# Kernel tuning notes

Hardware: AMD Instinct MI355X
Metric: run time of the kernel (lower is better)

Reference implementation:

```python
import jax, jax.numpy as jnp
import numpy as np

N = 50000      # nodes
E = 600000     # edges
IN = 128       # input_dim
HID = 128      # hidden_dim
OUT = 128      # output_dim
H = 4          # heads
D = OUT // H   # head dim
R = 4          # rel_num
L = 2          # n_layer
M = 10000      # len(idx)
EPS = 1e-5


def setup_inputs() -> dict:
    key = jax.random.key(0)
    ks = jax.random.split(key, 16)
    f = jax.random.normal
    inp = {
        "x": f(ks[0], (N, IN), jnp.float32),
        "proj_w": f(ks[1], (IN, HID), jnp.float32) / np.sqrt(IN).astype(np.float32),
        "proj_b": jnp.zeros((HID,), jnp.float32),
        "bn_gamma": jnp.ones((HID,), jnp.float32),
        "bn_beta": jnp.zeros((HID,), jnp.float32),
        # per-layer HGTConv params (stacked on leading L axis; layer0 in=HID, layer1 in=OUT, equal here)
        "q_w": f(ks[2], (L, HID, OUT), jnp.float32) / np.sqrt(HID).astype(np.float32),
        "q_b": jnp.zeros((L, OUT), jnp.float32),
        "k_w": f(ks[3], (L, HID, OUT), jnp.float32) / np.sqrt(HID).astype(np.float32),
        "k_b": jnp.zeros((L, OUT), jnp.float32),
        "v_w": f(ks[4], (L, HID, OUT), jnp.float32) / np.sqrt(HID).astype(np.float32),
        "v_b": jnp.zeros((L, OUT), jnp.float32),
        "a_w": f(ks[5], (L, OUT, OUT), jnp.float32) / np.sqrt(OUT).astype(np.float32),
        "a_b": jnp.zeros((L, OUT), jnp.float32),
        "skip": jnp.ones((L,), jnp.float32),
        "a_rel": f(ks[6], (L, R, H, D, D), jnp.float32) / np.sqrt(D).astype(np.float32),
        "m_rel": f(ks[7], (L, R, H, D, D), jnp.float32) / np.sqrt(D).astype(np.float32),
        "p_rel": jnp.ones((L, R, H), jnp.float32),
        "edge_index": jax.random.randint(ks[8], (2, E), 0, N, dtype=jnp.int32),
        "edge_type": jax.random.randint(ks[9], (E,), 0, R, dtype=jnp.int32),
        "idx": jax.random.randint(ks[10], (M,), 0, N, dtype=jnp.int32),
    }
    return inp


def _hgt_forward(x, proj_w, proj_b, bn_gamma, bn_beta, q_w, q_b, k_w, k_b, v_w, v_b,
                 a_w, a_b, skip, a_rel, m_rel, p_rel, edge_index, edge_type, idx):
    # proj + BatchNorm1d (training-mode batch statistics, biased variance)
    h = x @ proj_w + proj_b
    mu = h.mean(axis=0)
    var = jnp.mean((h - mu) ** 2, axis=0)
    h = (h - mu) * jax.lax.rsqrt(var + EPS) * bn_gamma + bn_beta

    src, dst = edge_index[0], edge_index[1]          # message from src(j) to dst(i)
    seg = dst * R + edge_type                        # per-(dst, relation) softmax segments
    scale = np.float32(1.0 / np.sqrt(D))

    for l in range(L):
        q = (h @ q_w[l] + q_b[l]).reshape(N, H, D)
        k = (h @ k_w[l] + k_b[l]).reshape(N, H, D)
        v = (h @ v_w[l] + v_b[l]).reshape(N, H, D)
        # relation-specific key/value transforms for every node/relation: [N,R,H,D]
        k_all = jnp.einsum('nhd,rhde->nrhe', k, a_rel[l])
        v_all = jnp.einsum('nhd,rhde->nrhe', v, m_rel[l])
        k_e = k_all[src, edge_type]                  # [E,H,D]
        v_e = v_all[src, edge_type]                  # [E,H,D]
        score = jnp.sum(q[dst] * k_e, axis=-1) * p_rel[l][edge_type] * scale  # [E,H]
        # per-relation segment softmax over incoming edges of each dst node
        smax = jax.ops.segment_max(score, seg, num_segments=N * R)
        e = jnp.exp(score - smax[seg])
        denom = jax.ops.segment_sum(e, seg, num_segments=N * R)
        alpha = e / denom[seg]                        # [E,H]
        out = jax.ops.segment_sum(alpha[..., None] * v_e, dst, num_segments=N)
        out = out.reshape(N, OUT)
        out = jax.nn.gelu(out, approximate=False) @ a_w[l] + a_b[l]
        b = jax.nn.sigmoid(skip[l])                   # learned skip gate
        h = b * out + (1.0 - b) * h                   # dims match -> residual mix
    return h[idx]


def reference(x, proj_w, proj_b, bn_gamma, bn_beta, q_w, q_b, k_w, k_b, v_w, v_b,
              a_w, a_b, skip, a_rel, m_rel, p_rel, edge_index, edge_type, idx):
    return _hgt_forward(x, proj_w, proj_b, bn_gamma, bn_beta, q_w, q_b, k_w, k_b,
                        v_w, v_b, a_w, a_b, skip, a_rel, m_rel, p_rel,
                        edge_index, edge_type, idx)
```

## Files before the change

kernel.cpp:

```cpp
#include <hip/hip_runtime.h>
#include <math.h>

#define NN 50000
#define EE 600000
#define MOUT 10000
#define DEGCAP 384
#define NT4 (NN * 4)

typedef short bf16x8 __attribute__((ext_vector_type(8)));
typedef float f32x4 __attribute__((ext_vector_type(4)));

__device__ __forceinline__ unsigned short f2bf(float x) {
    unsigned int u = __float_as_uint(x);
    u = (u + 0x7FFFu + ((u >> 16) & 1u)) >> 16;
    return (unsigned short)u;
}
__device__ __forceinline__ float bf2f(unsigned int b) {
    return __uint_as_float(b << 16);
}
__device__ __forceinline__ uint4 pack8bf(float4 a, float4 b) {
    uint4 r;
    r.x = (unsigned int)f2bf(a.x) | ((unsigned int)f2bf(a.y) << 16);
    r.y = (unsigned int)f2bf(a.z) | ((unsigned int)f2bf(a.w) << 16);
    r.z = (unsigned int)f2bf(b.x) | ((unsigned int)f2bf(b.y) << 16);
    r.w = (unsigned int)f2bf(b.z) | ((unsigned int)f2bf(b.w) << 16);
    return r;
}

__global__ __launch_bounds__(256) void prep_kernel(
    const float* __restrict__ proj_w, const float* __restrict__ a_w,
    const float* __restrict__ q_w, const float* __restrict__ q_b,
    const float* __restrict__ a_rel,
    const float* __restrict__ k_w, const float* __restrict__ k_b,
    const float* __restrict__ v_w, const float* __restrict__ v_b,
    const float* __restrict__ m_rel, const float* __restrict__ p_rel,
    unsigned short* __restrict__ wt_pa, unsigned short* __restrict__ qkvw,
    float* __restrict__ fbias, unsigned short* __restrict__ msg_wt,
    int* __restrict__ cnt, float* __restrict__ stats)
{
    const int b = blockIdx.x, t = threadIdx.x;
    if (b < 192) {
        int wi = b >> 6;
        int flat = (b & 63) * 256 + t;
        int n = flat >> 7, c = flat & 127;
        const float* src = (wi == 0) ? proj_w : (wi == 1) ? a_w : a_w + 16384;
        wt_pa[(size_t)wi * 16384 + n * 128 + c] = f2bf(src[c * 128 + n]);
    } else if (b < 960) {
        int q = b - 192;
        int l = q >= 384 ? 1 : 0;
        int flat = (q - l * 384) * 256 + t;
        int nrow = flat >> 7, c = flat & 127;
        unsigned short* wt = qkvw + (size_t)l * 98304;
        float* fb = fbias + l * 768;
        if (nrow < 512) {
            int r = nrow >> 7, hh = (nrow >> 5) & 3, d = nrow & 31;
            float prl = p_rel[l * 16 + r * 4 + hh] * 0.17677669529663687f;
            const float* qwc = q_w + (size_t)l * 16384 + c * 128 + hh * 32;
            const float* ar  = a_rel + (size_t)(l * 4 + r) * 4096 + hh * 1024 + d * 32;
            float s = 0.f;
            #pragma unroll 8
            for (int e = 0; e < 32; ++e) s += qwc[e] * ar[e];
            wt[(size_t)nrow * 128 + c] = f2bf(s * prl);
            if (c == 0) {
                const float* qb = q_b + l * 128 + hh * 32;
                float bb = 0.f;
                #pragma unroll 8
                for (int e = 0; e < 32; ++e) bb += qb[e] * ar[e];
                fb[nrow] = bb * prl;
            }
        } else {
            int j = nrow - 512;
            int tt = j >> 3, s = j & 7;
            int col = 4 * tt + (s & 3);
            const float* w  = (s < 4) ? k_w : v_w;
            const float* bb = (s < 4) ? k_b : v_b;
            wt[(size_t)nrow * 128 + c] = f2bf(w[(size_t)l * 16384 + c * 128 + col]);
            if (c == 0) fb[nrow] = bb[l * 128 + col];
        }
    } else if (b < 1472) {
        int q = b - 960;
        int l = q >= 256 ? 1 : 0;
        int flat = (q - l * 256) * 256 + t;
        int n = flat >> 9, kk = flat & 511;
        int h = n >> 5, e = n & 31;
        int r = kk >> 7, h2 = (kk >> 5) & 3, d = kk & 31;
        float val = (h2 == h) ? m_rel[(size_t)(l * 4 + r) * 4096 + h * 1024 + d * 32 + e] : 0.f;
        msg_wt[(size_t)l * 65536 + (size_t)n * 512 + kk] = f2bf(val);
    } else {
        int i = (b - 1472) * 256 + t;
        if (i < NT4) cnt[i] = 0;
        if (i < 256) stats[i] = 0.f;
    }
}

__global__ __launch_bounds__(256) void hist_kernel(const int* __restrict__ ei,
    const int* __restrict__ et, int* __restrict__ cnt, int E)
{
    int e = blockIdx.x * 256 + threadIdx.x;
    if (e < E) atomicAdd(&cnt[ei[E + e] * 4 + et[e]], 1);
}

__global__ __launch_bounds__(256) void scan_block_kernel(const int* __restrict__ cnt,
    int* __restrict__ excl, int* __restrict__ bsum, int n)
{
    __shared__ int tmp[256];
    int i = blockIdx.x * 256 + threadIdx.x;
    int v = (i < n) ? cnt[i] : 0;
    tmp[threadIdx.x] = v;
    __syncthreads();
    for (int ofs = 1; ofs < 256; ofs <<= 1) {
        int t = (threadIdx.x >= ofs) ? tmp[threadIdx.x - ofs] : 0;
        __syncthreads();
        tmp[threadIdx.x] += t;
        __syncthreads();
    }
    if (i < n) excl[i] = tmp[threadIdx.x] - v;
    if (threadIdx.x == 255) bsum[blockIdx.x] = tmp[255];
}

__global__ __launch_bounds__(256) void scan_add_kernel(int* __restrict__ excl,
    const int* __restrict__ bsum, int* __restrict__ fill,
    int* __restrict__ maskz, int n, int total)
{
    __shared__ int red[256];
    const int b = blockIdx.x;
    int partial = 0;
    for (int j = threadIdx.x; j < b; j += 256) partial += bsum[j];
    red[threadIdx.x] = partial;
    __syncthreads();
    for (int ofs = 128; ofs > 0; ofs >>= 1) {
        if (threadIdx.x < ofs) red[threadIdx.x] += red[threadIdx.x + ofs];
        __syncthreads();
    }
    int prefix = red[0];
    int i = b * 256 + threadIdx.x;
    if (i < n) {
        int o = excl[i] + prefix;
        excl[i] = o;
        fill[i] = o;
    }
    if (i < 12500) maskz[i] = 0;
    if (b == 0 && threadIdx.x == 0) excl[n] = total;
}

__global__ __launch_bounds__(256) void scatter_kernel(const int* __restrict__ ei,
    const int* __restrict__ et, int* __restrict__ fill, int* __restrict__ pack,
    const int* __restrict__ idxp, unsigned char* __restrict__ mask, int Mo, int E)
{
    int e = blockIdx.x * 256 + threadIdx.x;
    if (e >= E) return;
    int seg = ei[E + e] * 4 + et[e];
    int p = atomicAdd(&fill[seg], 1);
    pack[p] = ei[e];
    if (e < Mo) mask[idxp[e]] = 1;
}

__global__ __launch_bounds__(256) void projstats_kernel(
    const float* __restrict__ X, const unsigned short* __restrict__ Wt,
    const float* __restrict__ bias, unsigned short* __restrict__ Cb,
    float* __restrict__ stats, int M)
{
    __shared__ unsigned short As[128 * 40];
    __shared__ unsigned short Bs[128 * 40];
    const int t = threadIdx.x;
    const int wave = t >> 6, lane = t & 63;
    const int quad = lane >> 4, l16 = lane & 15;
    const int row0 = blockIdx.x * 128;
    const int wr = (wave & 1) * 64, wc = (wave >> 1) * 64;
    const int sr = t >> 1, sc = (t & 1) * 16;
    const int grow = row0 + sr;

    f32x4 acc[4][4];
    #pragma unroll
    for (int i = 0; i < 4; ++i)
        #pragma unroll
        for (int j = 0; j < 4; ++j)
            acc[i][j] = (f32x4){0.f, 0.f, 0.f, 0.f};

    uint4 av0 = make_uint4(0,0,0,0), av1 = av0, bv0, bv1;
    if (grow < M) {
        const float4* ap = (const float4*)(X + (size_t)grow * 128 + sc);
        av0 = pack8bf(ap[0], ap[1]);
        av1 = pack8bf(ap[2], ap[3]);
    }
    {
        const uint4* bp = (const uint4*)(Wt + (size_t)sr * 128 + sc);
        bv0 = bp[0]; bv1 = bp[1];
    }
    for (int it = 0; it < 4; ++it) {
        __syncthreads();
        *(uint4*)(As + sr * 40 + sc)     = av0;
        *(uint4*)(As + sr * 40 + sc + 8) = av1;
        *(uint4*)(Bs + sr * 40 + sc)     = bv0;
        *(uint4*)(Bs + sr * 40 + sc + 8) = bv1;
        __syncthreads();
        if (it + 1 < 4) {
            int kb = (it + 1) * 32;
            if (grow < M) {
                const float4* ap = (const float4*)(X + (size_t)grow * 128 + kb + sc);
                av0 = pack8bf(ap[0], ap[1]);
                av1 = pack8bf(ap[2], ap[3]);
            }
            const uint4* bp = (const uint4*)(Wt + (size_t)sr * 128 + kb + sc);
            bv0 = bp[0]; bv1 = bp[1];
        }
        bf16x8 af[4], bfr[4];
        #pragma unroll
        for (int f = 0; f < 4; ++f) {
            af[f]  = *(const bf16x8*)(As + (wr + f * 16 + l16) * 40 + quad * 8);
            bfr[f] = *(const bf16x8*)(Bs + (wc + f * 16 + l16) * 40 + quad * 8);
        }
        #pragma unroll
        for (int fr = 0; fr < 4; ++fr)
            #pragma unroll
            for (int fc = 0; fc < 4; ++fc)
                acc[fr][fc] = __builtin_amdgcn_mfma_f32_16x16x32_bf16(
                    af[fr], bfr[fc], acc[fr][fc], 0, 0, 0);
    }

    #pragma unroll
    for (int fc = 0; fc < 4; ++fc) {
        const int col = wc + fc * 16 + l16;
        const float bv = bias[col];
        float s = 0.f, s2 = 0.f;
        #pragma unroll
        for (int fr = 0; fr < 4; ++fr)
            #pragma unroll
            for (int reg = 0; reg < 4; ++reg) {
                int row = row0 + wr + fr * 16 + quad * 4 + reg;
                float val = acc[fr][fc][reg] + bv;
                if (row < M) {
                    Cb[(size_t)row * 128 + col] = f2bf(val);
                    s += val; s2 += val * val;
                }
            }
        s  += __shfl_xor(s, 16);  s  += __shfl_xor(s, 32);
        s2 += __shfl_xor(s2, 16); s2 += __shfl_xor(s2, 32);
        if (quad == 0) {
            atomicAdd(&stats[col], s);
            atomicAdd(&stats[128 + col], s2);
        }
    }
}

__global__ __launch_bounds__(256) void bnqkv_kernel(
    const unsigned short* __restrict__ hb, const float* __restrict__ stats,
    const float* __restrict__ gamma, const float* __restrict__ beta,
    const unsigned short* __restrict__ qkvw, const float* __restrict__ fbias,
    unsigned short* __restrict__ hn, unsigned short* __restrict__ qkv, int M)
{
    __shared__ unsigned short hS[128 * 136];
    __shared__ unsigned short Bs[128 * 40];
    __shared__ float mulS[128], addS[128];
    const int t = threadIdx.x;
    const int row0 = blockIdx.x * 128;
    if (t < 128) {
        float invN = 1.f / 50000.f;
        float mu = stats[t] * invN;
        float var = stats[128 + t] * invN - mu * mu;
        float ml = rsqrtf(var + 1e-5f) * gamma[t];
        mulS[t] = ml;
        addS[t] = beta[t] - mu * ml;
    }
    __syncthreads();
    #pragma unroll
    for (int u = 0; u < 8; ++u) {
        int li = t + u * 256;
        int row = li >> 4, c0 = (li & 15) * 8;
        uint4 pk = make_uint4(0, 0, 0, 0);
        if (row0 + row < M)
            pk = ((const uint4*)(hb + (size_t)(row0 + row) * 128))[li & 15];
        unsigned int w[4] = {pk.x, pk.y, pk.z, pk.w};
        uint4 o;
        unsigned int ov[4];
        #pragma unroll
        for (int g = 0; g < 4; ++g) {
            int c = c0 + g * 2;
            float a0 = bf2f(w[g] & 0xFFFFu) * mulS[c]     + addS[c];
            float a1 = bf2f(w[g] >> 16)     * mulS[c + 1] + addS[c + 1];
            ov[g] = (unsigned int)f2bf(a0) | ((unsigned int)f2bf(a1) << 16);
        }
        o.x = ov[0]; o.y = ov[1]; o.z = ov[2]; o.w = ov[3];
        *(uint4*)(hS + row * 136 + c0) = o;
        if (row0 + row < M)
            ((uint4*)(hn + (size_t)(row0 + row) * 128))[li & 15] = o;
    }
    __syncthreads();

    const int wave = t >> 6, lane = t & 63;
    const int quad = lane >> 4, l16 = lane & 15;
    const int wr = (wave & 1) * 64, wcl = (wave >> 1) * 64;
    const int sr = t >> 1, scc = (t & 1) * 16;

    uint4 pv0, pv1;
    {
        const uint4* bp = (const uint4*)(qkvw + (size_t)sr * 128 + scc);
        pv0 = bp[0]; pv1 = bp[1];
    }
    for (int ch = 0; ch < 6; ++ch) {
        f32x4 acc[4][4];
        #pragma unroll
        for (int i = 0; i < 4; ++i)
            #pragma unroll
            for (int j = 0; j < 4; ++j)
                acc[i][j] = (f32x4){0.f, 0.f, 0.f, 0.f};
        for (int it = 0; it < 4; ++it) {
            __syncthreads();
            *(uint4*)(Bs + sr * 40 + scc)     = pv0;
            *(uint4*)(Bs + sr * 40 + scc + 8) = pv1;
            __syncthreads();
            int nit = it + 1, nch = ch;
            if (nit == 4) { nit = 0; ++nch; }
            if (nch < 6) {
                const uint4* bp = (const uint4*)(qkvw + (size_t)(nch * 128 + sr) * 128 + nit * 32 + scc);
                pv0 = bp[0]; pv1 = bp[1];
            }
            bf16x8 af[4], bfr[4];
            #pragma unroll
            for (int f = 0; f < 4; ++f) {
                af[f]  = *(const bf16x8*)(hS + (wr + f * 16 + l16) * 136 + it * 32 + quad * 8);
                bfr[f] = *(const bf16x8*)(Bs + (wcl + f * 16 + l16) * 40 + quad * 8);
            }
            #pragma unroll
            for (int fr = 0; fr < 4; ++fr)
                #pragma unroll
                for (int fc = 0; fc < 4; ++fc)
                    acc[fr][fc] = __builtin_amdgcn_mfma_f32_16x16x32_bf16(
                        af[fr], bfr[fc], acc[fr][fc], 0, 0, 0);
        }
        float b4[4];
        #pragma unroll
        for (int fc = 0; fc < 4; ++fc)
            b4[fc] = fbias[ch * 128 + wcl + fc * 16 + l16];
        #pragma unroll
        for (int fr = 0; fr < 4; ++fr)
            #pragma unroll
            for (int reg = 0; reg < 4; ++reg) {
                int row = row0 + wr + fr * 16 + quad * 4 + reg;
                if (row >= M) continue;
                #pragma unroll
                for (int fc = 0; fc < 4; ++fc) {
                    int col = ch * 128 + wcl + fc * 16 + l16;
                    qkv[(size_t)row * 768 + col] = f2bf(acc[fr][fc][reg] + b4[fc]);
                }
            }
    }
}

__global__ __launch_bounds__(256) void agg_fused_kernel(
    const unsigned short* __restrict__ qkv,
    const unsigned short* __restrict__ qbuf, int qpitch,
    const int* __restrict__ off4, const int* __restrict__ pack,
    const int* __restrict__ rowmap, unsigned short* __restrict__ aggb, int count)
{
    __shared__ int spack[4][DEGCAP];
    const int wv = threadIdx.x >> 6;
    const int lane = threadIdx.x & 63;
    const int l32 = lane & 31;
    const int hi = lane >> 5;
    const int unit = blockIdx.x * 4 + wv;
    if (unit >= count) return;
    const int node = rowmap ? __builtin_amdgcn_readfirstlane(rowmap[unit]) : unit;

    const uint2* qrow = (const uint2*)(qbuf + (size_t)unit * qpitch);
    uint2 quv[4];
    #pragma unroll
    for (int r = 0; r < 4; ++r) quv[r] = qrow[r * 32 + l32];

    int off_r[5];
    #pragma unroll
    for (int i = 0; i < 5; ++i)
        off_r[i] = __builtin_amdgcn_readfirstlane(off4[node * 4 + i]);
    const int beg = off_r[0];
    const int deg = off_r[4] - beg;
    const bool cached = deg <= DEGCAP;

    if (cached) {
        for (int i = lane; i < deg; i += 64) spack[wv][i] = pack[beg + i];
        asm volatile("s_waitcnt vmcnt(0) lgkmcnt(0)" ::: "memory");
    }

    uint2 outw[4];
    #pragma unroll
    for (int r = 0; r < 4; ++r) {
        float q0 = bf2f(quv[r].x & 0xFFFFu), q1 = bf2f(quv[r].x >> 16);
        float q2 = bf2f(quv[r].y & 0xFFFFu), q3 = bf2f(quv[r].y >> 16);
        float den = 0.f, a0 = 0.f, a1 = 0.f, a2 = 0.f, a3 = 0.f;

        if (cached) {
            const int rb = off_r[r] - beg, re = off_r[r + 1] - beg;
            for (int i = rb; i < re; i += 4) {
                int i0 = i + hi;      if (i0 >= re) i0 = re - 1;
                int i1 = i + 2 + hi;  if (i1 >= re) i1 = re - 1;
                int s0 = spack[wv][i0], s1 = spack[wv][i1];
                uint4 kv0 = *(const uint4*)(qkv + (size_t)s0 * 768 + 512 + l32 * 8);
                uint4 kv1 = *(const uint4*)(qkv + (size_t)s1 * 768 + 512 + l32 * 8);
                {
                    float p = q0 * bf2f(kv0.x & 0xFFFFu) + q1 * bf2f(kv0.x >> 16)
                            + q2 * bf2f(kv0.y & 0xFFFFu) + q3 * bf2f(kv0.y >> 16);
                    p += __shfl_xor(p, 1); p += __shfl_xor(p, 2); p += __shfl_xor(p, 4);
                    float e = __expf(fminf(fmaxf(p, -80.f), 80.f));
                    if (i + hi >= re) e = 0.f;
                    den += e;
                    a0 += e * bf2f(kv0.z & 0xFFFFu); a1 += e * bf2f(kv0.z >> 16);
                    a2 += e * bf2f(kv0.w & 0xFFFFu); a3 += e * bf2f(kv0.w >> 16);
                }
                {
                    float p = q0 * bf2f(kv1.x & 0xFFFFu) + q1 * bf2f(kv1.x >> 16)
                            + q2 * bf2f(kv1.y & 0xFFFFu) + q3 * bf2f(kv1.y >> 16);
                    p += __shfl_xor(p, 1); p += __shfl_xor(p, 2); p += __shfl_xor(p, 4);
                    float e = __expf(fminf(fmaxf(p, -80.f), 80.f));
                    if (i + 2 + hi >= re) e = 0.f;
                    den += e;
                    a0 += e * bf2f(kv1.z & 0xFFFFu); a1 += e * bf2f(kv1.z >> 16);
                    a2 += e * bf2f(kv1.w & 0xFFFFu); a3 += e * bf2f(kv1.w >> 16);
                }
            }
        } else {
            const int pe_end = off_r[r + 1];
            for (int pp = off_r[r]; pp < pe_end; pp += 2) {
                int pe = pp + hi; if (pe >= pe_end) pe = pe_end - 1;
                int src = pack[pe];
                uint4 kv = *(const uint4*)(qkv + (size_t)src * 768 + 512 + l32 * 8);
                float p = q0 * bf2f(kv.x & 0xFFFFu) + q1 * bf2f(kv.x >> 16)
                        + q2 * bf2f(kv.y & 0xFFFFu) + q3 * bf2f(kv.y >> 16);
                p += __shfl_xor(p, 1); p += __shfl_xor(p, 2); p += __shfl_xor(p, 4);
                float e = __expf(fminf(fmaxf(p, -80.f), 80.f));
                if (pp + hi >= pe_end) e = 0.f;
                den += e;
                a0 += e * bf2f(kv.z & 0xFFFFu); a1 += e * bf2f(kv.z >> 16);
                a2 += e * bf2f(kv.w & 0xFFFFu); a3 += e * bf2f(kv.w >> 16);
            }
        }
        den += __shfl_xor(den, 32);
        a0  += __shfl_xor(a0, 32);
        a1  += __shfl_xor(a1, 32);
        a2  += __shfl_xor(a2, 32);
        a3  += __shfl_xor(a3, 32);
        float inv = den > 0.f ? 1.f / den : 0.f;
        outw[r].x = (unsigned int)f2bf(a0 * inv) | ((unsigned int)f2bf(a1 * inv) << 16);
        outw[r].y = (unsigned int)f2bf(a2 * inv) | ((unsigned int)f2bf(a3 * inv) << 16);
    }
    if (hi == 0) {
        uint2* op = (uint2*)(aggb + (size_t)unit * 512);
        #pragma unroll
        for (int r = 0; r < 4; ++r) op[r * 32 + l32] = outw[r];
    }
}

__global__ __launch_bounds__(256) void mlpqkv_kernel(
    const unsigned short* __restrict__ A, const unsigned short* __restrict__ W3t,
    const unsigned short* __restrict__ AWt, const float* __restrict__ a_bias,
    const float* __restrict__ skipv, const unsigned short* __restrict__ hres,
    const unsigned short* __restrict__ qkvw1, const float* __restrict__ fbias1,
    const unsigned char* __restrict__ mask,
    unsigned short* __restrict__ h1, unsigned short* __restrict__ qkv, int M)
{
    __shared__ unsigned short As[128 * 40];
    __shared__ unsigned short Bs[128 * 40];
    __shared__ unsigned short msgS[128 * 136];
    const int t = threadIdx.x;
    const int wave = t >> 6, lane = t & 63;
    const int quad = lane >> 4, l16 = lane & 15;
    const int row0 = blockIdx.x * 128;
    const int wr = (wave & 1) * 64, wcl = (wave >> 1) * 64;
    const int sr = t >> 1, scc = (t & 1) * 16;
    const int grow = row0 + sr;
    const bool rvalid = grow < M;

    f32x4 acc[4][4];
    #pragma unroll
    for (int i = 0; i < 4; ++i)
        #pragma unroll
        for (int j = 0; j < 4; ++j)
            acc[i][j] = (f32x4){0.f, 0.f, 0.f, 0.f};

    uint4 av0 = make_uint4(0,0,0,0), av1 = av0, bv0, bv1;
    if (rvalid) {
        const uint4* ap = (const uint4*)(A + (size_t)grow * 512 + scc);
        av0 = ap[0]; av1 = ap[1];
    }
    {
        const uint4* bp = (const uint4*)(W3t + (size_t)sr * 512 + scc);
        bv0 = bp[0]; bv1 = bp[1];
    }
    for (int it = 0; it < 16; ++it) {
        __syncthreads();
        *(uint4*)(As + sr * 40 + scc)     = av0;
        *(uint4*)(As + sr * 40 + scc + 8) = av1;
        *(uint4*)(Bs + sr * 40 + scc)     = bv0;
        *(uint4*)(Bs + sr * 40 + scc + 8) = bv1;
        __syncthreads();
        if (it + 1 < 16) {
            int kb = (it + 1) * 32;
            if (rvalid) {
                const uint4* ap = (const uint4*)(A + (size_t)grow * 512 + kb + scc);
                av0 = ap[0]; av1 = ap[1];
            }
            const uint4* bp = (const uint4*)(W3t + (size_t)sr * 512 + kb + scc);
            bv0 = bp[0]; bv1 = bp[1];
        }
        bf16x8 af[4], bfr[4];
        #pragma unroll
        for (int f = 0; f < 4; ++f) {
            af[f]  = *(const bf16x8*)(As + (wr + f * 16 + l16) * 40 + quad * 8);
            bfr[f] = *(const bf16x8*)(Bs + (wcl + f * 16 + l16) * 40 + quad * 8);
        }
        #pragma unroll
        for (int fr = 0; fr < 4; ++fr)
            #pragma unroll
            for (int fc = 0; fc < 4; ++fc)
                acc[fr][fc] = __builtin_amdgcn_mfma_f32_16x16x32_bf16(
                    af[fr], bfr[fc], acc[fr][fc], 0, 0, 0);
    }

    #pragma unroll
    for (int fr = 0; fr < 4; ++fr)
        #pragma unroll
        for (int reg = 0; reg < 4; ++reg) {
            int rl = wr + fr * 16 + quad * 4 + reg;
            #pragma unroll
            for (int fc = 0; fc < 4; ++fc) {
                int col = wcl + fc * 16 + l16;
                float v = acc[fr][fc][reg];
                float gl = 0.5f * v * (1.f + erff(v * 0.70710678118654752f));
                msgS[rl * 136 + col] = f2bf(gl);
            }
        }

    f32x4 acc2[4][4];
    #pragma unroll
    for (int i = 0; i < 4; ++i)
        #pragma unroll
        for (int j = 0; j < 4; ++j)
            acc2[i][j] = (f32x4){0.f, 0.f, 0.f, 0.f};
    uint4 pv0, pv1;
    {
        const uint4* bp = (const uint4*)(AWt + (size_t)sr * 128 + scc);
        pv0 = bp[0]; pv1 = bp[1];
    }
    for (int it = 0; it < 4; ++it) {
        __syncthreads();
        *(uint4*)(Bs + sr * 40 + scc)     = pv0;
        *(uint4*)(Bs + sr * 40 + scc + 8) = pv1;
        __syncthreads();
        if (it + 1 < 4) {
            const uint4* bp = (const uint4*)(AWt + (size_t)sr * 128 + (it + 1) * 32 + scc);
            pv0 = bp[0]; pv1 = bp[1];
        } else {
            const uint4* bp = (const uint4*)(qkvw1 + (size_t)(4 * 128 + sr) * 128 + scc);
            pv0 = bp[0]; pv1 = bp[1];
        }
        bf16x8 af[4], bfr[4];
        #pragma unroll
        for (int f = 0; f < 4; ++f) {
            af[f]  = *(const bf16x8*)(msgS + (wr + f * 16 + l16) * 136 + it * 32 + quad * 8);
            bfr[f] = *(const bf16x8*)(Bs + (wcl + f * 16 + l16) * 40 + quad * 8);
        }
        #pragma unroll
        for (int fr = 0; fr < 4; ++fr)
            #pragma unroll
            for (int fc = 0; fc < 4; ++fc)
                acc2[fr][fc] = __builtin_amdgcn_mfma_f32_16x16x32_bf16(
                    af[fr], bfr[fc], acc2[fr][fc], 0, 0, 0);
    }

    const float gate = 1.f / (1.f + __expf(-skipv[0]));
    __syncthreads();
    #pragma unroll
    for (int fr = 0; fr < 4; ++fr)
        #pragma unroll
        for (int reg = 0; reg < 4; ++reg) {
            int rl = wr + fr * 16 + quad * 4 + reg;
            int row = row0 + rl;
            const bool rv = row < M;
            const bool mw = rv && mask[row];
            #pragma unroll
            for (int fc = 0; fc < 4; ++fc) {
                int col = wcl + fc * 16 + l16;
                float val = acc2[fr][fc][reg] + a_bias[col];
                float nv = val;
                if (rv) {
                    unsigned int hu = hres[(size_t)row * 128 + col];
                    nv = gate * val + (1.f - gate) * bf2f(hu);
                    if (mw) h1[(size_t)row * 128 + col] = f2bf(nv);
                }
                msgS[rl * 136 + col] = f2bf(nv);
            }
        }

    for (int ch = 4; ch < 6; ++ch) {
        f32x4 acc3[4][4];
        #pragma unroll
        for (int i = 0; i < 4; ++i)
            #pragma unroll
            for (int j = 0; j < 4; ++j)
                acc3[i][j] = (f32x4){0.f, 0.f, 0.f, 0.f};
        for (int it = 0; it < 4; ++it) {
            __syncthreads();
            *(uint4*)(Bs + sr * 40 + scc)     = pv0;
            *(uint4*)(Bs + sr * 40 + scc + 8) = pv1;
            __syncthreads();
            int nit = it + 1, nch = ch;
            if (nit == 4) { nit = 0; ++nch; }
            if (nch < 6) {
                const uint4* bp = (const uint4*)(qkvw1 + (size_t)(nch * 128 + sr) * 128 + nit * 32 + scc);
                pv0 = bp[0]; pv1 = bp[1];
            }
            bf16x8 af[4], bfr[4];
            #pragma unroll
            for (int f = 0; f < 4; ++f) {
                af[f]  = *(const bf16x8*)(msgS + (wr + f * 16 + l16) * 136 + it * 32 + quad * 8);
                bfr[f] = *(const bf16x8*)(Bs + (wcl + f * 16 + l16) * 40 + quad * 8);
            }
            #pragma unroll
            for (int fr = 0; fr < 4; ++fr)
                #pragma unroll
                for (int fc = 0; fc < 4; ++fc)
                    acc3[fr][fc] = __builtin_amdgcn_mfma_f32_16x16x32_bf16(
                        af[fr], bfr[fc], acc3[fr][fc], 0, 0, 0);
        }
        float b4[4];
        #pragma unroll
        for (int fc = 0; fc < 4; ++fc)
            b4[fc] = fbias1[ch * 128 + wcl + fc * 16 + l16];
        #pragma unroll
        for (int fr = 0; fr < 4; ++fr)
            #pragma unroll
            for (int reg = 0; reg < 4; ++reg) {
                int row = row0 + wr + fr * 16 + quad * 4 + reg;
                if (row >= M) continue;
                #pragma unroll
                for (int fc = 0; fc < 4; ++fc) {
                    int col = ch * 128 + wcl + fc * 16 + l16;
                    qkv[(size_t)row * 768 + col] = f2bf(acc3[fr][fc][reg] + b4[fc]);
                }
            }
    }
}

__global__ __launch_bounds__(256) void q1_kernel(
    const unsigned short* __restrict__ h1, const int* __restrict__ idxp,
    const unsigned short* __restrict__ qkvw1, const float* __restrict__ fbias1,
    unsigned short* __restrict__ q1, int M)
{
    __shared__ unsigned short hS[128 * 136];
    __shared__ unsigned short Bs[128 * 40];
    const int t = threadIdx.x;
    const int row0 = blockIdx.x * 128;
    #pragma unroll
    for (int u = 0; u < 8; ++u) {
        int li = t + u * 256;
        int row = li >> 4, c = li & 15;
        uint4 pk = make_uint4(0, 0, 0, 0);
        if (row0 + row < M) {
            int node = idxp[row0 + row];
            pk = ((const uint4*)(h1 + (size_t)node * 128))[c];
        }
        *(uint4*)(hS + row * 136 + c * 8) = pk;
    }
    __syncthreads();

    const int wave = t >> 6, lane = t & 63;
    const int quad = lane >> 4, l16 = lane & 15;
    const int wr = (wave & 1) * 64, wcl = (wave >> 1) * 64;
    const int sr = t >> 1, scc = (t & 1) * 16;
    uint4 pv0, pv1;
    {
        const uint4* bp = (const uint4*)(qkvw1 + (size_t)sr * 128 + scc);
        pv0 = bp[0]; pv1 = bp[1];
    }
    for (int ch = 0; ch < 4; ++ch) {
        f32x4 acc[4][4];
        #pragma unroll
        for (int i = 0; i < 4; ++i)
            #pragma unroll
            for (int j = 0; j < 4; ++j)
                acc[i][j] = (f32x4){0.f, 0.f, 0.f, 0.f};
        for (int it = 0; it < 4; ++it) {
            __syncthreads();
            *(uint4*)(Bs + sr * 40 + scc)     = pv0;
            *(uint4*)(Bs + sr * 40 + scc + 8) = pv1;
            __syncthreads();
            int nit = it + 1, nch = ch;
            if (nit == 4) { nit = 0; ++nch; }
            if (nch < 4) {
                const uint4* bp = (const uint4*)(qkvw1 + (size_t)(nch * 128 + sr) * 128 + nit * 32 + scc);
                pv0 = bp[0]; pv1 = bp[1];
            }
            bf16x8 af[4], bfr[4];
            #pragma unroll
            for (int f = 0; f < 4; ++f) {
                af[f]  = *(const bf16x8*)(hS + (wr + f * 16 + l16) * 136 + it * 32 + quad * 8);
                bfr[f] = *(const bf16x8*)(Bs + (wcl + f * 16 + l16) * 40 + quad * 8);
            }
            #pragma unroll
            for (int fr = 0; fr < 4; ++fr)
                #pragma unroll
                for (int fc = 0; fc < 4; ++fc)
                    acc[fr][fc] = __builtin_amdgcn_mfma_f32_16x16x32_bf16(
                        af[fr], bfr[fc], acc[fr][fc], 0, 0, 0);
        }
        float b4[4];
        #pragma unroll
        for (int fc = 0; fc < 4; ++fc)
            b4[fc] = fbias1[ch * 128 + wcl + fc * 16 + l16];
        #pragma unroll
        for (int fr = 0; fr < 4; ++fr)
            #pragma unroll
            for (int reg = 0; reg < 4; ++reg) {
                int row = row0 + wr + fr * 16 + quad * 4 + reg;
                if (row >= M) continue;
                #pragma unroll
                for (int fc = 0; fc < 4; ++fc) {
                    int col = ch * 128 + wcl + fc * 16 + l16;
                    q1[(size_t)row * 512 + col] = f2bf(acc[fr][fc][reg] + b4[fc]);
                }
            }
    }
}

__global__ __launch_bounds__(256) void mlp1_kernel(
    const unsigned short* __restrict__ A, const unsigned short* __restrict__ W3t,
    const unsigned short* __restrict__ AWt, const float* __restrict__ a_bias,
    const float* __restrict__ skipv, const unsigned short* __restrict__ hres,
    const int* __restrict__ rowmap, float* __restrict__ out, int M)
{
    __shared__ unsigned short As[128 * 40];
    __shared__ unsigned short Bs[128 * 40];
    __shared__ unsigned short msgS[128 * 136];
    const int t = threadIdx.x;
    const int wave = t >> 6, lane = t & 63;
    const int quad = lane >> 4, l16 = lane & 15;
    const int row0 = blockIdx.x * 128;
    const int wr = (wave & 1) * 64, wcl = (wave >> 1) * 64;
    const int sr = t >> 1, scc = (t & 1) * 16;
    const int grow = row0 + sr;
    const bool rvalid = grow < M;

    f32x4 acc[4][4];
    #pragma unroll
    for (int i = 0; i < 4; ++i)
        #pragma unroll
        for (int j = 0; j < 4; ++j)
            acc[i][j] = (f32x4){0.f, 0.f, 0.f, 0.f};

    uint4 av0 = make_uint4(0,0,0,0), av1 = av0, bv0, bv1;
    if (rvalid) {
        const uint4* ap = (const uint4*)(A + (size_t)grow * 512 + scc);
        av0 = ap[0]; av1 = ap[1];
    }
    {
        const uint4* bp = (const uint4*)(W3t + (size_t)sr * 512 + scc);
        bv0 = bp[0]; bv1 = bp[1];
    }
    for (int it = 0; it < 16; ++it) {
        __syncthreads();
        *(uint4*)(As + sr * 40 + scc)     = av0;
        *(uint4*)(As + sr * 40 + scc + 8) = av1;
        *(uint4*)(Bs + sr * 40 + scc)     = bv0;
        *(uint4*)(Bs + sr * 40 + scc + 8) = bv1;
        __syncthreads();
        if (it + 1 < 16) {
            int kb = (it + 1) * 32;
            if (rvalid) {
                const uint4* ap = (const uint4*)(A + (size_t)grow * 512 + kb + scc);
                av0 = ap[0]; av1 = ap[1];
            }
            const uint4* bp = (const uint4*)(W3t + (size_t)sr * 512 + kb + scc);
            bv0 = bp[0]; bv1 = bp[1];
        }
        bf16x8 af[4], bfr[4];
        #pragma unroll
        for (int f = 0; f < 4; ++f) {
            af[f]  = *(const bf16x8*)(As + (wr + f * 16 + l16) * 40 + quad * 8);
            bfr[f] = *(const bf16x8*)(Bs + (wcl + f * 16 + l16) * 40 + quad * 8);
        }
        #pragma unroll
        for (int fr = 0; fr < 4; ++fr)
            #pragma unroll
            for (int fc = 0; fc < 4; ++fc)
                acc[fr][fc] = __builtin_amdgcn_mfma_f32_16x16x32_bf16(
                    af[fr], bfr[fc], acc[fr][fc], 0, 0, 0);
    }

    #pragma unroll
    for (int fr = 0; fr < 4; ++fr)
        #pragma unroll
        for (int reg = 0; reg < 4; ++reg) {
            int rl = wr + fr * 16 + quad * 4 + reg;
            #pragma unroll
            for (int fc = 0; fc < 4; ++fc) {
                int col = wcl + fc * 16 + l16;
                float v = acc[fr][fc][reg];
                float gl = 0.5f * v * (1.f + erff(v * 0.70710678118654752f));
                msgS[rl * 136 + col] = f2bf(gl);
            }
        }

    f32x4 acc2[4][4];
    #pragma unroll
    for (int i = 0; i < 4; ++i)
        #pragma unroll
        for (int j = 0; j < 4; ++j)
            acc2[i][j] = (f32x4){0.f, 0.f, 0.f, 0.f};
    uint4 pv0, pv1;
    {
        const uint4* bp = (const uint4*)(AWt + (size_t)sr * 128 + scc);
        pv0 = bp[0]; pv1 = bp[1];
    }
    for (int it = 0; it < 4; ++it) {
        __syncthreads();
        *(uint4*)(Bs + sr * 40 + scc)     = pv0;
        *(uint4*)(Bs + sr * 40 + scc + 8) = pv1;
        __syncthreads();
        if (it + 1 < 4) {
            const uint4* bp = (const uint4*)(AWt + (size_t)sr * 128 + (it + 1) * 32 + scc);
            pv0 = bp[0]; pv1 = bp[1];
        }
        bf16x8 af[4], bfr[4];
        #pragma unroll
        for (int f = 0; f < 4; ++f) {
            af[f]  = *(const bf16x8*)(msgS + (wr + f * 16 + l16) * 136 + it * 32 + quad * 8);
            bfr[f] = *(const bf16x8*)(Bs + (wcl + f * 16 + l16) * 40 + quad * 8);
        }
        #pragma unroll
        for (int fr = 0; fr < 4; ++fr)
            #pragma unroll
            for (int fc = 0; fc < 4; ++fc)
                acc2[fr][fc] = __builtin_amdgcn_mfma_f32_16x16x32_bf16(
                    af[fr], bfr[fc], acc2[fr][fc], 0, 0, 0);
    }

    const float gate = 1.f / (1.f + __expf(-skipv[0]));
    #pragma unroll
    for (int fr = 0; fr < 4; ++fr)
        #pragma unroll
        for (int reg = 0; reg < 4; ++reg) {
            int row = row0 + wr + fr * 16 + quad * 4 + reg;
            if (row >= M) continue;
            int hrow = rowmap[row];
            #pragma unroll
            for (int fc = 0; fc < 4; ++fc) {
                int col = wcl + fc * 16 + l16;
                float val = acc2[fr][fc][reg] + a_bias[col];
                float nv = gate * val + (1.f - gate) * bf2f((unsigned int)hres[(size_t)hrow * 128 + col]);
                out[(size_t)row * 128 + col] = nv;
            }
        }
}

extern "C" void kernel_launch(void* const* d_in, const int* in_sizes, int n_in,
                              void* d_out, int out_size, void* d_ws, size_t ws_size,
                              hipStream_t stream)
{
    const float* x      = (const float*)d_in[0];
    const float* proj_w = (const float*)d_in[1];
    const float* proj_b = (const float*)d_in[2];
    const float* bn_g   = (const float*)d_in[3];
    const float* bn_b   = (const float*)d_in[4];
    const float* q_w    = (const float*)d_in[5];
    const float* q_b    = (const float*)d_in[6];
    const float* k_w    = (const float*)d_in[7];
    const float* k_b    = (const float*)d_in[8];
    const float* v_w    = (const float*)d_in[9];
    const float* v_b    = (const float*)d_in[10];
    const float* a_w    = (const float*)d_in[11];
    const float* a_b    = (const float*)d_in[12];
    const float* skip   = (const float*)d_in[13];
    const float* a_rel  = (const float*)d_in[14];
    const float* m_rel  = (const float*)d_in[15];
    const float* p_rel  = (const float*)d_in[16];
    const int* edge_index = (const int*)d_in[17];
    const int* edge_type  = (const int*)d_in[18];
    const int* idx        = (const int*)d_in[19];
    float* out = (float*)d_out;

    const int N = NN, E = EE;
    float* ws = (float*)d_ws;
    size_t o = 0;
    float* stats  = ws + o;  o += 256;
    float* fbias  = ws + o;  o += 2 * 768;
    int* cnt  = (int*)(ws + o); o += NT4;
    int* off4 = (int*)(ws + o); o += NT4 + 1;
    int* fill = (int*)(ws + o); o += NT4;
    int* bsum = (int*)(ws + o); o += 1024;
    int* pack = (int*)(ws + o); o += E;
    unsigned short* x_bf   = (unsigned short*)(ws + o); o += (size_t)N * 64;
    unsigned short* h_bf   = (unsigned short*)(ws + o); o += (size_t)N * 64;
    unsigned short* hn_bf  = (unsigned short*)(ws + o); o += (size_t)N * 64;
    unsigned short* h1_bf  = (unsigned short*)(ws + o); o += (size_t)N * 64;
    unsigned short* qkv_bf = (unsigned short*)(ws + o); o += (size_t)N * 384;
    unsigned short* agg_bf = (unsigned short*)(ws + o); o += (size_t)N * 256;
    unsigned short* wt_pa  = (unsigned short*)(ws + o); o += 3 * 16384 / 2;
    unsigned short* qkvw   = (unsigned short*)(ws + o); o += 2 * 98304 / 2;
    unsigned short* msg_wt = (unsigned short*)(ws + o); o += 2 * 65536 / 2;

    unsigned char* mask = (unsigned char*)cnt;
    unsigned short* q1 = x_bf;

    const int NB4 = (NT4 + 255) / 256;
    const int g = (N + 127) / 128;

    prep_kernel<<<1472 + NB4, 256, 0, stream>>>(
        proj_w, a_w, q_w, q_b, a_rel, k_w, k_b, v_w, v_b, m_rel, p_rel,
        wt_pa, qkvw, fbias, msg_wt, cnt, stats);

    hist_kernel<<<(E + 255) / 256, 256, 0, stream>>>(edge_index, edge_type, cnt, E);
    scan_block_kernel<<<NB4, 256, 0, stream>>>(cnt, off4, bsum, NT4);
    scan_add_kernel<<<NB4, 256, 0, stream>>>(off4, bsum, fill, cnt, NT4, E);
    scatter_kernel<<<(E + 255) / 256, 256, 0, stream>>>(edge_index, edge_type, fill,
                                                        pack, idx, mask, MOUT, E);

    projstats_kernel<<<g, 256, 0, stream>>>(x, wt_pa, proj_b, h_bf, stats, N);

    bnqkv_kernel<<<g, 256, 0, stream>>>(h_bf, stats, bn_g, bn_b, qkvw, fbias,
                                        hn_bf, qkv_bf, N);

    agg_fused_kernel<<<(N + 3) / 4, 256, 0, stream>>>(qkv_bf, qkv_bf, 768,
                                                      off4, pack, nullptr, agg_bf, N);

    mlpqkv_kernel<<<g, 256, 0, stream>>>(agg_bf, msg_wt, wt_pa + 16384, a_b, skip,
                                         hn_bf, qkvw + 98304, fbias + 768,
                                         mask, h1_bf, qkv_bf, N);

    q1_kernel<<<(MOUT + 127) / 128, 256, 0, stream>>>(h1_bf, idx, qkvw + 98304,
                                                      fbias + 768, q1, MOUT);

    agg_fused_kernel<<<(MOUT + 3) / 4, 256, 0, stream>>>(qkv_bf, q1, 512,
                                                         off4, pack, idx, agg_bf, MOUT);

    mlp1_kernel<<<(MOUT + 127) / 128, 256, 0, stream>>>(agg_bf, msg_wt + 65536,
                                                        wt_pa + 2 * 16384, a_b + 128,
                                                        skip + 1, h1_bf, idx, out, MOUT);
}
```

Baseline: 442.5 us.

## Exploit block-diagonal relation message weights to cut MFMA work fourfold

The message-transform GEMM used a dense 512x128 weight that was zero outside head-diagonal blocks. The new layout stores only the per-relation 128x32 compact blocks, and the GEMM loop runs 4 relation iterations of K=32 instead of 16. Each wave selects the A columns for its own heads from a full 128-column slab staged in shared memory, which removes the As buffer and three quarters of the MFMAs and weight loads. The cost is larger per-thread register staging (8 uint4 per iteration) and an extra barrier before the reused msgS buffer is overwritten.

```diff
diff --git a/kernel.cpp b/kernel.cpp
--- a/kernel.cpp
+++ b/kernel.cpp
@@ -77,17 +77,16 @@
             wt[(size_t)nrow * 128 + c] = f2bf(w[(size_t)l * 16384 + c * 128 + col]);
             if (c == 0) fb[nrow] = bb[l * 128 + col];
         }
-    } else if (b < 1472) {
+    } else if (b < 1088) {
         int q = b - 960;
-        int l = q >= 256 ? 1 : 0;
-        int flat = (q - l * 256) * 256 + t;
-        int n = flat >> 9, kk = flat & 511;
-        int h = n >> 5, e = n & 31;
-        int r = kk >> 7, h2 = (kk >> 5) & 3, d = kk & 31;
-        float val = (h2 == h) ? m_rel[(size_t)(l * 4 + r) * 4096 + h * 1024 + d * 32 + e] : 0.f;
-        msg_wt[(size_t)l * 65536 + (size_t)n * 512 + kk] = f2bf(val);
+        int l = q >= 64 ? 1 : 0;
+        int flat = (q - l * 64) * 256 + t;
+        int r = flat >> 12, rem = flat & 4095;
+        int n = rem >> 5, d = rem & 31;
+        float val = m_rel[(size_t)(l * 4 + r) * 4096 + (n >> 5) * 1024 + d * 32 + (n & 31)];
+        msg_wt[(size_t)l * 16384 + r * 4096 + n * 32 + d] = f2bf(val);
     } else {
-        int i = (b - 1472) * 256 + t;
+        int i = (b - 1088) * 256 + t;
         if (i < NT4) cnt[i] = 0;
         if (i < 256) stats[i] = 0.f;
     }
@@ -449,14 +448,13 @@
 }
 
 __global__ __launch_bounds__(256) void mlpqkv_kernel(
-    const unsigned short* __restrict__ A, const unsigned short* __restrict__ W3t,
+    const unsigned short* __restrict__ A, const unsigned short* __restrict__ W3c,
     const unsigned short* __restrict__ AWt, const float* __restrict__ a_bias,
     const float* __restrict__ skipv, const unsigned short* __restrict__ hres,
     const unsigned short* __restrict__ qkvw1, const float* __restrict__ fbias1,
     const unsigned char* __restrict__ mask,
     unsigned short* __restrict__ h1, unsigned short* __restrict__ qkv, int M)
 {
-    __shared__ unsigned short As[128 * 40];
     __shared__ unsigned short Bs[128 * 40];
     __shared__ unsigned short msgS[128 * 136];
     const int t = threadIdx.x;
@@ -465,8 +463,10 @@
     const int row0 = blockIdx.x * 128;
     const int wr = (wave & 1) * 64, wcl = (wave >> 1) * 64;
     const int sr = t >> 1, scc = (t & 1) * 16;
+    const int scc2 = (t & 1) * 64;
     const int grow = row0 + sr;
     const bool rvalid = grow < M;
+    const int h2b = wcl >> 5;
 
     f32x4 acc[4][4];
     #pragma unroll
@@ -475,44 +475,53 @@
         for (int j = 0; j < 4; ++j)
             acc[i][j] = (f32x4){0.f, 0.f, 0.f, 0.f};
 
-    uint4 av0 = make_uint4(0,0,0,0), av1 = av0, bv0, bv1;
+    uint4 av[8];
+    #pragma unroll
+    for (int j = 0; j < 8; ++j) av[j] = make_uint4(0, 0, 0, 0);
     if (rvalid) {
-        const uint4* ap = (const uint4*)(A + (size_t)grow * 512 + scc);
-        av0 = ap[0]; av1 = ap[1];
-    }
+        const uint4* ap = (const uint4*)(A + (size_t)grow * 512 + scc2);
+        #pragma unroll
+        for (int j = 0; j < 8; ++j) av[j] = ap[j];
+    }
+    uint4 bw0, bw1;
     {
-        const uint4* bp = (const uint4*)(W3t + (size_t)sr * 512 + scc);
-        bv0 = bp[0]; bv1 = bp[1];
-    }
-    for (int it = 0; it < 16; ++it) {
-        __syncthreads();
-        *(uint4*)(As + sr * 40 + scc)     = av0;
-        *(uint4*)(As + sr * 40 + scc + 8) = av1;
-        *(uint4*)(Bs + sr * 40 + scc)     = bv0;
-        *(uint4*)(Bs + sr * 40 + scc + 8) = bv1;
-        __syncthreads();
-        if (it + 1 < 16) {
-            int kb = (it + 1) * 32;
+        const uint4* bp = (const uint4*)(W3c + sr * 32 + scc);
+        bw0 = bp[0]; bw1 = bp[1];
+    }
+    for (int it = 0; it < 4; ++it) {
+        __syncthreads();
+        #pragma unroll
+        for (int j = 0; j < 8; ++j)
+            *(uint4*)(msgS + sr * 136 + scc2 + j * 8) = av[j];
+        *(uint4*)(Bs + sr * 40 + scc)     = bw0;
+        *(uint4*)(Bs + sr * 40 + scc + 8) = bw1;
+        __syncthreads();
+        if (it + 1 < 4) {
             if (rvalid) {
-                const uint4* ap = (const uint4*)(A + (size_t)grow * 512 + kb + scc);
-                av0 = ap[0]; av1 = ap[1];
-            }
-            const uint4* bp = (const uint4*)(W3t + (size_t)sr * 512 + kb + scc);
-            bv0 = bp[0]; bv1 = bp[1];
-        }
-        bf16x8 af[4], bfr[4];
-        #pragma unroll
-        for (int f = 0; f < 4; ++f) {
-            af[f]  = *(const bf16x8*)(As + (wr + f * 16 + l16) * 40 + quad * 8);
+                const uint4* ap = (const uint4*)(A + (size_t)grow * 512 + (it + 1) * 128 + scc2);
+                #pragma unroll
+                for (int j = 0; j < 8; ++j) av[j] = ap[j];
+            }
+            const uint4* bp = (const uint4*)(W3c + (it + 1) * 4096 + sr * 32 + scc);
+            bw0 = bp[0]; bw1 = bp[1];
+        }
+        bf16x8 af2[2][4], bfr[4];
+        #pragma unroll
+        for (int g = 0; g < 2; ++g)
+            #pragma unroll
+            for (int f = 0; f < 4; ++f)
+                af2[g][f] = *(const bf16x8*)(msgS + (wr + f * 16 + l16) * 136 + (h2b + g) * 32 + quad * 8);
+        #pragma unroll
+        for (int f = 0; f < 4; ++f)
             bfr[f] = *(const bf16x8*)(Bs + (wcl + f * 16 + l16) * 40 + quad * 8);
-        }
         #pragma unroll
         for (int fr = 0; fr < 4; ++fr)
             #pragma unroll
             for (int fc = 0; fc < 4; ++fc)
                 acc[fr][fc] = __builtin_amdgcn_mfma_f32_16x16x32_bf16(
-                    af[fr], bfr[fc], acc[fr][fc], 0, 0, 0);
-    }
+                    af2[fc >> 1][fr], bfr[fc], acc[fr][fc], 0, 0, 0);
+    }
+    __syncthreads();
 
     #pragma unroll
     for (int fr = 0; fr < 4; ++fr)
@@ -721,12 +730,11 @@
 }
 
 __global__ __launch_bounds__(256) void mlp1_kernel(
-    const unsigned short* __restrict__ A, const unsigned short* __restrict__ W3t,
+    const unsigned short* __restrict__ A, const unsigned short* __restrict__ W3c,
     const unsigned short* __restrict__ AWt, const float* __restrict__ a_bias,
     const float* __restrict__ skipv, const unsigned short* __restrict__ hres,
     const int* __restrict__ rowmap, float* __restrict__ out, int M)
 {
-    __shared__ unsigned short As[128 * 40];
     __shared__ unsigned short Bs[128 * 40];
     __shared__ unsigned short msgS[128 * 136];
     const int t = threadIdx.x;
@@ -735,8 +743,10 @@
     const int row0 = blockIdx.x * 128;
     const int wr = (wave & 1) * 64, wcl = (wave >> 1) * 64;
     const int sr = t >> 1, scc = (t & 1) * 16;
+    const int scc2 = (t & 1) * 64;
     const int grow = row0 + sr;
     const bool rvalid = grow < M;
+    const int h2b = wcl >> 5;
 
     f32x4 acc[4][4];
     #pragma unroll
@@ -745,44 +755,53 @@
         for (int j = 0; j < 4; ++j)
             acc[i][j] = (f32x4){0.f, 0.f, 0.f, 0.f};
 
-    uint4 av0 = make_uint4(0,0,0,0), av1 = av0, bv0, bv1;
+    uint4 av[8];
+    #pragma unroll
+    for (int j = 0; j < 8; ++j) av[j] = make_uint4(0, 0, 0, 0);
     if (rvalid) {
-        const uint4* ap = (const uint4*)(A + (size_t)grow * 512 + scc);
-        av0 = ap[0]; av1 = ap[1];
-    }
+        const uint4* ap = (const uint4*)(A + (size_t)grow * 512 + scc2);
+        #pragma unroll
+        for (int j = 0; j < 8; ++j) av[j] = ap[j];
+    }
+    uint4 bw0, bw1;
     {
-        const uint4* bp = (const uint4*)(W3t + (size_t)sr * 512 + scc);
-        bv0 = bp[0]; bv1 = bp[1];
-    }
-    for (int it = 0; it < 16; ++it) {
-        __syncthreads();
-        *(uint4*)(As + sr * 40 + scc)     = av0;
-        *(uint4*)(As + sr * 40 + scc + 8) = av1;
-        *(uint4*)(Bs + sr * 40 + scc)     = bv0;
-        *(uint4*)(Bs + sr * 40 + scc + 8) = bv1;
-        __syncthreads();
-        if (it + 1 < 16) {
-            int kb = (it + 1) * 32;
+        const uint4* bp = (const uint4*)(W3c + sr * 32 + scc);
+        bw0 = bp[0]; bw1 = bp[1];
+    }
+    for (int it = 0; it < 4; ++it) {
+        __syncthreads();
+        #pragma unroll
+        for (int j = 0; j < 8; ++j)
+            *(uint4*)(msgS + sr * 136 + scc2 + j * 8) = av[j];
+        *(uint4*)(Bs + sr * 40 + scc)     = bw0;
+        *(uint4*)(Bs + sr * 40 + scc + 8) = bw1;
+        __syncthreads();
+        if (it + 1 < 4) {
             if (rvalid) {
-                const uint4* ap = (const uint4*)(A + (size_t)grow * 512 + kb + scc);
-                av0 = ap[0]; av1 = ap[1];
-            }
-            const uint4* bp = (const uint4*)(W3t + (size_t)sr * 512 + kb + scc);
-            bv0 = bp[0]; bv1 = bp[1];
-        }
-        bf16x8 af[4], bfr[4];
-        #pragma unroll
-        for (int f = 0; f < 4; ++f) {
-            af[f]  = *(const bf16x8*)(As + (wr + f * 16 + l16) * 40 + quad * 8);
+                const uint4* ap = (const uint4*)(A + (size_t)grow * 512 + (it + 1) * 128 + scc2);
+                #pragma unroll
+                for (int j = 0; j < 8; ++j) av[j] = ap[j];
+            }
+            const uint4* bp = (const uint4*)(W3c + (it + 1) * 4096 + sr * 32 + scc);
+            bw0 = bp[0]; bw1 = bp[1];
+        }
+        bf16x8 af2[2][4], bfr[4];
+        #pragma unroll
+        for (int g = 0; g < 2; ++g)
+            #pragma unroll
+            for (int f = 0; f < 4; ++f)
+                af2[g][f] = *(const bf16x8*)(msgS + (wr + f * 16 + l16) * 136 + (h2b + g) * 32 + quad * 8);
+        #pragma unroll
+        for (int f = 0; f < 4; ++f)
             bfr[f] = *(const bf16x8*)(Bs + (wcl + f * 16 + l16) * 40 + quad * 8);
-        }
         #pragma unroll
         for (int fr = 0; fr < 4; ++fr)
             #pragma unroll
             for (int fc = 0; fc < 4; ++fc)
                 acc[fr][fc] = __builtin_amdgcn_mfma_f32_16x16x32_bf16(
-                    af[fr], bfr[fc], acc[fr][fc], 0, 0, 0);
-    }
+                    af2[fc >> 1][fr], bfr[fc], acc[fr][fc], 0, 0, 0);
+    }
+    __syncthreads();
 
     #pragma unroll
     for (int fr = 0; fr < 4; ++fr)
@@ -902,7 +921,7 @@
     const int NB4 = (NT4 + 255) / 256;
     const int g = (N + 127) / 128;
 
-    prep_kernel<<<1472 + NB4, 256, 0, stream>>>(
+    prep_kernel<<<1088 + NB4, 256, 0, stream>>>(
         proj_w, a_w, q_w, q_b, a_rel, k_w, k_b, v_w, v_b, m_rel, p_rel,
         wt_pa, qkvw, fbias, msg_wt, cnt, stats);
 
@@ -930,7 +949,7 @@
     agg_fused_kernel<<<(MOUT + 3) / 4, 256, 0, stream>>>(qkv_bf, q1, 512,
                                                          off4, pack, idx, agg_bf, MOUT);
 
-    mlp1_kernel<<<(MOUT + 127) / 128, 256, 0, stream>>>(agg_bf, msg_wt + 65536,
+    mlp1_kernel<<<(MOUT + 127) / 128, 256, 0, stream>>>(agg_bf, msg_wt + 16384,
                                                         wt_pa + 2 * 16384, a_b + 128,
                                                         skip + 1, h1_bf, idx, out, MOUT);
 }
```

New measurement: 434.4 us. About the same (-1.8%).
